# Kernel tuning notes

Hardware: AMD Instinct MI355X
Metric: run time of the kernel (lower is better)

Reference implementation:

```python
import jax, jax.numpy as jnp
import numpy as np

V, E, H, L, T, B = 30522, 256, 256, 512, 64, 128
EOS = 2


def setup_inputs() -> dict:
    key = jax.random.key(0)
    ks = jax.random.split(key, 16)
    s = 0.05
    return {
        "z": jax.random.normal(ks[0], (B, L), jnp.float32),
        "target_seq": jax.random.randint(ks[1], (B, T), 0, V, jnp.int64),
        "emb": jax.random.normal(ks[2], (V, E), jnp.float32) * s,
        "W_ih0": jax.random.normal(ks[3], (4 * H, E), jnp.float32) * s,
        "W_hh0": jax.random.normal(ks[4], (4 * H, H), jnp.float32) * s,
        "b_ih0": jax.random.normal(ks[5], (4 * H,), jnp.float32) * s,
        "b_hh0": jax.random.normal(ks[6], (4 * H,), jnp.float32) * s,
        "W_ih1": jax.random.normal(ks[7], (4 * H, H), jnp.float32) * s,
        "W_hh1": jax.random.normal(ks[8], (4 * H, H), jnp.float32) * s,
        "b_ih1": jax.random.normal(ks[9], (4 * H,), jnp.float32) * s,
        "b_hh1": jax.random.normal(ks[10], (4 * H,), jnp.float32) * s,
        "W_out": jax.random.normal(ks[11], (V, H), jnp.float32) * s,
        "b_out": jax.random.normal(ks[12], (V,), jnp.float32) * s,
        "W_lat": jax.random.normal(ks[13], (H, L), jnp.float32) * s,
        "b_lat": jax.random.normal(ks[14], (H,), jnp.float32) * s,
    }


def _lstm_cell(x, h, c, W_ih, W_hh, b_ih, b_hh):
    # PyTorch gate order: i, f, g, o
    gates = x @ W_ih.T + b_ih + h @ W_hh.T + b_hh  # [B, 4H]
    i, f, g, o = jnp.split(gates, 4, axis=-1)
    i, f, o = jax.nn.sigmoid(i), jax.nn.sigmoid(f), jax.nn.sigmoid(o)
    g = jnp.tanh(g)
    c_new = f * c + i * g
    h_new = o * jnp.tanh(c_new)
    return h_new, c_new


def reference(z, target_seq, emb, W_ih0, W_hh0, b_ih0, b_hh0,
              W_ih1, W_hh1, b_ih1, b_hh1, W_out, b_out, W_lat, b_lat):
    batch = z.shape[0]
    # initial hidden from latent, repeated per layer; cell zeros
    h_init = z @ W_lat.T + b_lat  # [B, H]
    c_init = jnp.zeros_like(h_init)
    # teacher-forced input tokens: [EOS, target[:, :-1]]
    tok = jnp.concatenate(
        [jnp.full((batch, 1), EOS, target_seq.dtype), target_seq[:, :-1]], axis=1)
    xs = emb[tok]  # [B, T, E]
    xs = jnp.transpose(xs, (1, 0, 2))  # [T, B, E]

    def step(carry, x_t):
        h0, c0, h1, c1 = carry
        h0, c0 = _lstm_cell(x_t, h0, c0, W_ih0, W_hh0, b_ih0, b_hh0)
        h1, c1 = _lstm_cell(h0, h1, c1, W_ih1, W_hh1, b_ih1, b_hh1)
        return (h0, c0, h1, c1), h1

    _, hs = jax.lax.scan(step, (h_init, c_init, h_init, c_init), xs)  # [T, B, H]
    logits = jnp.einsum('tbh,vh->btv', hs, W_out) + b_out  # [B, T, V]
    return logits
```

## Files before the change

### kernel.cpp

```cpp
#include <hip/hip_runtime.h>
#include <hip/hip_bf16.h>

#define B_ 128
#define T_ 64
#define H_ 256
#define E_ 256
#define L_ 512
#define V_ 30522
#define EOS_ 2
#define BH_ (B_ * H_)

typedef __attribute__((ext_vector_type(8))) short bf16x8;
typedef __attribute__((ext_vector_type(4))) float f32x4;

__device__ __forceinline__ float4 ld4(const float* p) { return *(const float4*)p; }
__device__ __forceinline__ float dot4(float4 a, float4 b) {
  return a.x * b.x + a.y * b.y + a.z * b.z + a.w * b.w;
}
__device__ __forceinline__ float sigf(float x) {
  return __builtin_amdgcn_rcpf(1.f + __expf(-x));
}
__device__ __forceinline__ float tanh_fast(float x) {
  float e = __expf(2.f * x);
  return 1.f - 2.f * __builtin_amdgcn_rcpf(e + 1.f);
}
__device__ __forceinline__ f32x4 mfma16(bf16x8 a, bf16x8 b, f32x4 c) {
  return __builtin_amdgcn_mfma_f32_16x16x32_bf16(a, b, c, 0, 0, 0);
}

__global__ __launch_bounds__(256) void conv_all(
    const float* __restrict__ emb, const float* __restrict__ w0i,
    const float* __restrict__ w0h, const float* __restrict__ w1i,
    const float* __restrict__ w1h, const float* __restrict__ wout,
    __hip_bfloat16* __restrict__ dEmb, __hip_bfloat16* __restrict__ dW0i,
    __hip_bfloat16* __restrict__ dW0h, __hip_bfloat16* __restrict__ dW1i,
    __hip_bfloat16* __restrict__ dW1h, __hip_bfloat16* __restrict__ dWout) {
  long i = ((long)blockIdx.x * 256 + threadIdx.x) * 8;
  const float* src; __hip_bfloat16* dst; long off;
  if (i < 7813632L)       { src = emb;  dst = dEmb;  off = i; }
  else if (i < 8075776L)  { src = w0i;  dst = dW0i;  off = i - 7813632L; }
  else if (i < 8337920L)  { src = w0h;  dst = dW0h;  off = i - 8075776L; }
  else if (i < 8600064L)  { src = w1i;  dst = dW1i;  off = i - 8337920L; }
  else if (i < 8862208L)  { src = w1h;  dst = dW1h;  off = i - 8600064L; }
  else if (i < 16675840L) { src = wout; dst = dWout; off = i - 8862208L; }
  else return;
  float4 lo = ld4(src + off), hi = ld4(src + off + 4);
  union { bf16x8 v8; __hip_bfloat16 e[8]; } u;
  u.e[0] = __float2bfloat16(lo.x); u.e[1] = __float2bfloat16(lo.y);
  u.e[2] = __float2bfloat16(lo.z); u.e[3] = __float2bfloat16(lo.w);
  u.e[4] = __float2bfloat16(hi.x); u.e[5] = __float2bfloat16(hi.y);
  u.e[6] = __float2bfloat16(hi.z); u.e[7] = __float2bfloat16(hi.w);
  *(bf16x8*)(dst + off) = u.v8;
}

__global__ __launch_bounds__(256) void reset_cnt(int* __restrict__ c) {
  int i = blockIdx.x * 256 + threadIdx.x;
  if (i < 8448) c[i] = 0;
}

__global__ __launch_bounds__(256) void init_kernel(
    const float* __restrict__ z, const float* __restrict__ W_lat,
    const float* __restrict__ b_lat,
    __hip_bfloat16* __restrict__ h0hi, __hip_bfloat16* __restrict__ h0res,
    __hip_bfloat16* __restrict__ hshi, __hip_bfloat16* __restrict__ hsres) {
  int b = blockIdx.x;
  int h = threadIdx.x;
  const float* zr = z + (size_t)b * L_;
  const float* wr = W_lat + (size_t)h * L_;
  float acc = b_lat[h];
  #pragma unroll 4
  for (int l = 0; l < L_; l += 4) acc += dot4(ld4(zr + l), ld4(wr + l));
  __hip_bfloat16 hi = __float2bfloat16(acc);
  __hip_bfloat16 re = __float2bfloat16(acc - __bfloat162float(hi));
  int idx = b * H_ + h;
  h0hi[idx] = hi; h0res[idx] = re;
  hshi[idx] = hi; hsres[idx] = re;
}

__global__ __launch_bounds__(256, 1) void lstm_persist(
    const int* __restrict__ targ, const __hip_bfloat16* __restrict__ embB,
    const __hip_bfloat16* __restrict__ Wih0B, const __hip_bfloat16* __restrict__ Whh0B,
    const float* __restrict__ b_ih0, const float* __restrict__ b_hh0,
    const __hip_bfloat16* __restrict__ Wih1B, const __hip_bfloat16* __restrict__ Whh1B,
    const float* __restrict__ b_ih1, const float* __restrict__ b_hh1,
    __hip_bfloat16* __restrict__ h0hi, __hip_bfloat16* __restrict__ h0res,
    __hip_bfloat16* __restrict__ hshi, __hip_bfloat16* __restrict__ hsres,
    int* __restrict__ flags, int* __restrict__ tickets) {
  __shared__ int role_sh;
  __shared__ int gang_sh;
  if (threadIdx.x == 0) {
    unsigned xcd;
    asm volatile("s_getreg_b32 %0, hwreg(HW_REG_XCC_ID)" : "=s"(xcd));
    xcd &= 7u;
    role_sh = __hip_atomic_fetch_add(tickets + xcd * 32, 1, __ATOMIC_RELAXED,
                                     __HIP_MEMORY_SCOPE_AGENT);
    gang_sh = (int)xcd;
  }
  __syncthreads();
  const int role = role_sh;
  if (role >= 32) return;
  const int gang = gang_sh;
  const bool isL0 = role < 16;
  const int chunk = role & 15;

  int* flag0 = flags + gang * 1024;
  int* flag1 = flag0 + 512;

  const int tid = threadIdx.x;
  const int lane = tid & 63;
  const int wave = tid >> 6;
  const int arow = lane & 15;
  const int klo = lane >> 4;
  const int hcol = chunk * 16 + arow;
  const int brow0 = gang * 16;
  const int myrow = brow0 + arow;

  const __hip_bfloat16* W1 = isL0 ? Wih0B : Wih1B;
  const __hip_bfloat16* W2 = isL0 ? Whh0B : Whh1B;
  bf16x8 bw1[8], bw2[8];
  {
    const size_t wrow = (size_t)(wave * 256 + hcol) * 256;
    #pragma unroll
    for (int ks = 0; ks < 8; ++ks) {
      bw1[ks] = *(const bf16x8*)(W1 + wrow + ks * 32 + klo * 8);
      bw2[ks] = *(const bf16x8*)(W2 + wrow + ks * 32 + klo * 8);
    }
  }

  const int erow = tid >> 4;
  const int ecol = tid & 15;
  const float* bi = isL0 ? b_ih0 : b_ih1;
  const float* bh = isL0 ? b_hh0 : b_hh1;
  const int ehcol = chunk * 16 + ecol;
  const float bias_i = bi[ehcol] + bh[ehcol];
  const float bias_f = bi[256 + ehcol] + bh[256 + ehcol];
  const float bias_g = bi[512 + ehcol] + bh[512 + ehcol];
  const float bias_o = bi[768 + ehcol] + bh[768 + ehcol];
  float c_state = 0.f;

  __shared__ float glds[4][16][17];

  for (int t = 0; t < T_; ++t) {
    {
      const int need0 = isL0 ? t : t + 1;
      const int need1 = isL0 ? 0 : t;
      if (tid < 64) {
        int* p = nullptr; int need = 0;
        if (lane < 16) { p = flag0 + lane * 32; need = need0; }
        else if (lane < 32) { p = flag1 + (lane - 16) * 32; need = need1; }
        int it = 0;
        for (;;) {
          bool ok = true;
          if (p && need > 0) ok = (atomicAdd(p, 0) >= need);
          if (__all(ok)) break;
          if (++it >= (1 << 14)) break;
          __builtin_amdgcn_s_sleep(1);
        }
      }
      __syncthreads();
    }

    f32x4 acc0 = (f32x4){0.f, 0.f, 0.f, 0.f};
    f32x4 acc1 = (f32x4){0.f, 0.f, 0.f, 0.f};
    if (isL0) {
      int tok = (t == 0) ? EOS_ : targ[myrow * T_ + t - 1];
      const __hip_bfloat16* xp = embB + (size_t)tok * E_;
      const __hip_bfloat16* hhp = h0hi + (size_t)t * BH_ + myrow * H_;
      const __hip_bfloat16* hrp = h0res + (size_t)t * BH_ + myrow * H_;
      #pragma unroll
      for (int ks = 0; ks < 8; ++ks) {
        const int ko = ks * 32 + klo * 8;
        bf16x8 ax = *(const bf16x8*)(xp + ko);
        bf16x8 ahh = *(const bf16x8*)(hhp + ko);
        bf16x8 ahr = *(const bf16x8*)(hrp + ko);
        if (ks & 1) {
          acc1 = mfma16(ax, bw1[ks], acc1);
          acc1 = mfma16(ahh, bw2[ks], acc1);
          acc1 = mfma16(ahr, bw2[ks], acc1);
        } else {
          acc0 = mfma16(ax, bw1[ks], acc0);
          acc0 = mfma16(ahh, bw2[ks], acc0);
          acc0 = mfma16(ahr, bw2[ks], acc0);
        }
      }
    } else {
      const __hip_bfloat16* xhp = h0hi + (size_t)(t + 1) * BH_ + myrow * H_;
      const __hip_bfloat16* xrp = h0res + (size_t)(t + 1) * BH_ + myrow * H_;
      const __hip_bfloat16* hhp = hshi + (size_t)t * BH_ + myrow * H_;
      const __hip_bfloat16* hrp = hsres + (size_t)t * BH_ + myrow * H_;
      #pragma unroll
      for (int ks = 0; ks < 8; ++ks) {
        const int ko = ks * 32 + klo * 8;
        bf16x8 axh = *(const bf16x8*)(xhp + ko);
        bf16x8 axr = *(const bf16x8*)(xrp + ko);
        bf16x8 ahh = *(const bf16x8*)(hhp + ko);
        bf16x8 ahr = *(const bf16x8*)(hrp + ko);
        if (ks & 1) {
          acc1 = mfma16(axh, bw1[ks], acc1);
          acc1 = mfma16(axr, bw1[ks], acc1);
          acc1 = mfma16(ahh, bw2[ks], acc1);
          acc1 = mfma16(ahr, bw2[ks], acc1);
        } else {
          acc0 = mfma16(axh, bw1[ks], acc0);
          acc0 = mfma16(axr, bw1[ks], acc0);
          acc0 = mfma16(ahh, bw2[ks], acc0);
          acc0 = mfma16(ahr, bw2[ks], acc0);
        }
      }
    }
    #pragma unroll
    for (int r = 0; r < 4; ++r)
      glds[wave][klo * 4 + r][arow] = acc0[r] + acc1[r];
    __syncthreads();

    {
      float gi = glds[0][erow][ecol] + bias_i;
      float gf = glds[1][erow][ecol] + bias_f;
      float gg = glds[2][erow][ecol] + bias_g;
      float go = glds[3][erow][ecol] + bias_o;
      float iv = sigf(gi), fv = sigf(gf), gv = tanh_fast(gg), ov = sigf(go);
      c_state = fv * c_state + iv * gv;
      float h = ov * tanh_fast(c_state);
      __hip_bfloat16 hi = __float2bfloat16(h);
      __hip_bfloat16 re = __float2bfloat16(h - __bfloat162float(hi));
      size_t off = (size_t)(t + 1) * BH_ + (size_t)(brow0 + erow) * H_ + ehcol;
      (isL0 ? h0hi : hshi)[off] = hi;
      (isL0 ? h0res : hsres)[off] = re;
    }

    __syncthreads();
    if (tid == 0) atomicAdd((isL0 ? flag0 : flag1) + chunk * 32, 1);
  }
}

__global__ __launch_bounds__(256) void gemm_out(
    const __hip_bfloat16* __restrict__ hs,
    const __hip_bfloat16* __restrict__ Wb, const float* __restrict__ bout,
    float* __restrict__ out) {
  __shared__ __hip_bfloat16 ldsA[2][128 * 32];
  __shared__ __hip_bfloat16 ldsB[2][128 * 32];

  const int tid = threadIdx.x;
  const int lane = tid & 63;
  const int wave = tid >> 6;
  const int wr = wave >> 1, wc = wave & 1;
  const int m0 = blockIdx.x * 128;
  const int n0 = blockIdx.y * 128;
  const int row_in = lane & 15;
  const int kgrp = lane >> 4;

  auto stage = [&](int kb, int buf) {
    #pragma unroll
    for (int p = 0; p < 2; ++p) {
      int slot = p * 256 + wave * 64 + lane;
      int row = slot >> 2;
      int kd = ((slot & 3) + (row >> 1)) & 3;
      const __hip_bfloat16* srcA = hs + (size_t)(m0 + row) * H_ + kb * 32 + kd * 8;
      int rn = n0 + row; if (rn >= V_) rn = V_ - 1;
      const __hip_bfloat16* srcB = Wb + (size_t)rn * H_ + kb * 32 + kd * 8;
      __hip_bfloat16* dstA = &ldsA[buf][0] + (p * 2048 + wave * 512);
      __hip_bfloat16* dstB = &ldsB[buf][0] + (p * 2048 + wave * 512);
      __builtin_amdgcn_global_load_lds(
          (const __attribute__((address_space(1))) unsigned int*)srcA,
          (__attribute__((address_space(3))) unsigned int*)dstA, 16, 0, 0);
      __builtin_amdgcn_global_load_lds(
          (const __attribute__((address_space(1))) unsigned int*)srcB,
          (__attribute__((address_space(3))) unsigned int*)dstB, 16, 0, 0);
    }
  };

  f32x4 acc[4][4];
  #pragma unroll
  for (int i = 0; i < 4; ++i)
    #pragma unroll
    for (int j = 0; j < 4; ++j) acc[i][j] = (f32x4){0.f, 0.f, 0.f, 0.f};

  stage(0, 0);
  __syncthreads();

  int buf = 0;
  for (int kb = 0; kb < 8; ++kb) {
    if (kb < 7) stage(kb + 1, buf ^ 1);
    bf16x8 a[4], b[4];
    #pragma unroll
    for (int mi = 0; mi < 4; ++mi) {
      int row = wr * 64 + mi * 16 + row_in;
      int g = (kgrp - (row >> 1)) & 3;
      a[mi] = *(const bf16x8*)(&ldsA[buf][0] + row * 32 + g * 8);
    }
    #pragma unroll
    for (int ni = 0; ni < 4; ++ni) {
      int row = wc * 64 + ni * 16 + row_in;
      int g = (kgrp - (row >> 1)) & 3;
      b[ni] = *(const bf16x8*)(&ldsB[buf][0] + row * 32 + g * 8);
    }
    #pragma unroll
    for (int mi = 0; mi < 4; ++mi)
      #pragma unroll
      for (int ni = 0; ni < 4; ++ni)
        acc[mi][ni] = mfma16(a[mi], b[ni], acc[mi][ni]);
    __syncthreads();
    buf ^= 1;
  }

  #pragma unroll
  for (int ni = 0; ni < 4; ++ni) {
    int v = n0 + wc * 64 + ni * 16 + row_in;
    if (v >= V_) continue;
    float bias = bout[v];
    #pragma unroll
    for (int mi = 0; mi < 4; ++mi) {
      #pragma unroll
      for (int r = 0; r < 4; ++r) {
        int m = m0 + wr * 64 + mi * 16 + kgrp * 4 + r;
        int tt = m >> 7;
        int bb_ = m & 127;
        out[((size_t)bb_ * T_ + tt) * V_ + v] = acc[mi][ni][r] + bias;
      }
    }
  }
}

extern "C" void kernel_launch(void* const* d_in, const int* in_sizes, int n_in,
                              void* d_out, int out_size, void* d_ws, size_t ws_size,
                              hipStream_t stream) {
  const float* z     = (const float*)d_in[0];
  const int*   targ  = (const int*)d_in[1];
  const float* emb   = (const float*)d_in[2];
  const float* W_ih0 = (const float*)d_in[3];
  const float* W_hh0 = (const float*)d_in[4];
  const float* b_ih0 = (const float*)d_in[5];
  const float* b_hh0 = (const float*)d_in[6];
  const float* W_ih1 = (const float*)d_in[7];
  const float* W_hh1 = (const float*)d_in[8];
  const float* b_ih1 = (const float*)d_in[9];
  const float* b_hh1 = (const float*)d_in[10];
  const float* W_out = (const float*)d_in[11];
  const float* b_out = (const float*)d_in[12];
  const float* W_lat = (const float*)d_in[13];
  const float* b_lat = (const float*)d_in[14];
  float* out = (float*)d_out;

  char* ws = (char*)d_ws;
  __hip_bfloat16* h0hi  = (__hip_bfloat16*)(ws);
  __hip_bfloat16* h0res = (__hip_bfloat16*)(ws + 4259840);
  __hip_bfloat16* hshi  = (__hip_bfloat16*)(ws + 8519680);
  __hip_bfloat16* hsres = (__hip_bfloat16*)(ws + 12779520);
  __hip_bfloat16* embB  = (__hip_bfloat16*)(ws + 17039360);
  __hip_bfloat16* Wih0B = (__hip_bfloat16*)(ws + 32666624);
  __hip_bfloat16* Whh0B = (__hip_bfloat16*)(ws + 33190912);
  __hip_bfloat16* Wih1B = (__hip_bfloat16*)(ws + 33715200);
  __hip_bfloat16* Whh1B = (__hip_bfloat16*)(ws + 34239488);
  __hip_bfloat16* WoutB = (__hip_bfloat16*)(ws + 34763776);
  int* flags = (int*)(ws + 50391040);
  int* tickets = flags + 8192;

  reset_cnt<<<33, 256, 0, stream>>>(flags);
  conv_all<<<8144, 256, 0, stream>>>(emb, W_ih0, W_hh0, W_ih1, W_hh1, W_out,
                                     embB, Wih0B, Whh0B, Wih1B, Whh1B, WoutB);
  init_kernel<<<128, 256, 0, stream>>>(z, W_lat, b_lat, h0hi, h0res, hshi, hsres);

  lstm_persist<<<512, 256, 0, stream>>>(
      targ, embB,
      Wih0B, Whh0B, b_ih0, b_hh0,
      Wih1B, Whh1B, b_ih1, b_hh1,
      h0hi, h0res, hshi, hsres, flags, tickets);

  {
    dim3 g(64, 239);
    gemm_out<<<g, 256, 0, stream>>>(hshi + BH_, WoutB, b_out, out);
  }
}
```

Measured before the change: 1.055 ms.

## Fuse LSTM recurrence and output projection into one persistent kernel with flag-gated tiles

Merges the persistent LSTM kernel and the vocabulary projection GEMM into a single launch. Blocks beyond the 32 recurrence roles per XCD pull output tiles from a per-XCD work queue, each tile covering 8 timesteps by 16 batch rows by 128 vocab columns. Before computing, a tile spin-waits on per-timestep completion counters that the layer-1 blocks increment. This lets the large logits GEMM overlap the serial recurrence instead of running after it. In exchange it adds spin-waiting, sharing of compute units with the latency-critical recurrence blocks, and a dependence on enough blocks being co-resident.

Result: faster. 950.7 us (-9.9%).

```diff
diff --git a/kernel.cpp b/kernel.cpp
--- a/kernel.cpp
+++ b/kernel.cpp
@@ -9,6 +9,8 @@
 #define V_ 30522
 #define EOS_ 2
 #define BH_ (B_ * H_)
+#define NTILE_N 239
+#define TILES_PER_XCD (8 * NTILE_N)
 
 typedef __attribute__((ext_vector_type(8))) short bf16x8;
 typedef __attribute__((ext_vector_type(4))) float f32x4;
@@ -55,7 +57,7 @@
 
 __global__ __launch_bounds__(256) void reset_cnt(int* __restrict__ c) {
   int i = blockIdx.x * 256 + threadIdx.x;
-  if (i < 8448) c[i] = 0;
+  if (i < 25088) c[i] = 0;
 }
 
 __global__ __launch_bounds__(256) void init_kernel(
@@ -77,7 +79,7 @@
   hshi[idx] = hi; hsres[idx] = re;
 }
 
-__global__ __launch_bounds__(256, 1) void lstm_persist(
+__global__ __launch_bounds__(256, 3) void fused(
     const int* __restrict__ targ, const __hip_bfloat16* __restrict__ embB,
     const __hip_bfloat16* __restrict__ Wih0B, const __hip_bfloat16* __restrict__ Whh0B,
     const float* __restrict__ b_ih0, const float* __restrict__ b_hh0,
@@ -85,10 +87,15 @@
     const float* __restrict__ b_ih1, const float* __restrict__ b_hh1,
     __hip_bfloat16* __restrict__ h0hi, __hip_bfloat16* __restrict__ h0res,
     __hip_bfloat16* __restrict__ hshi, __hip_bfloat16* __restrict__ hsres,
-    int* __restrict__ flags, int* __restrict__ tickets) {
-  __shared__ int role_sh;
-  __shared__ int gang_sh;
-  if (threadIdx.x == 0) {
+    const __hip_bfloat16* __restrict__ Wb, const float* __restrict__ bout,
+    float* __restrict__ out,
+    int* __restrict__ flags, int* __restrict__ tickets,
+    int* __restrict__ gqx, int* __restrict__ hsdone_g) {
+  __shared__ int role_sh, gang_sh, tile_sh;
+  __shared__ char smem[32768];
+
+  const int tid = threadIdx.x;
+  if (tid == 0) {
     unsigned xcd;
     asm volatile("s_getreg_b32 %0, hwreg(HW_REG_XCC_ID)" : "=s"(xcd));
     xcd &= 7u;
@@ -98,224 +105,244 @@
   }
   __syncthreads();
   const int role = role_sh;
-  if (role >= 32) return;
   const int gang = gang_sh;
-  const bool isL0 = role < 16;
-  const int chunk = role & 15;
-
-  int* flag0 = flags + gang * 1024;
-  int* flag1 = flag0 + 512;
-
-  const int tid = threadIdx.x;
   const int lane = tid & 63;
-  const int wave = tid >> 6;
-  const int arow = lane & 15;
-  const int klo = lane >> 4;
-  const int hcol = chunk * 16 + arow;
-  const int brow0 = gang * 16;
-  const int myrow = brow0 + arow;
-
-  const __hip_bfloat16* W1 = isL0 ? Wih0B : Wih1B;
-  const __hip_bfloat16* W2 = isL0 ? Whh0B : Whh1B;
-  bf16x8 bw1[8], bw2[8];
-  {
-    const size_t wrow = (size_t)(wave * 256 + hcol) * 256;
-    #pragma unroll
-    for (int ks = 0; ks < 8; ++ks) {
-      bw1[ks] = *(const bf16x8*)(W1 + wrow + ks * 32 + klo * 8);
-      bw2[ks] = *(const bf16x8*)(W2 + wrow + ks * 32 + klo * 8);
+
+  if (role < 32) {
+    const bool isL0 = role < 16;
+    const int chunk = role & 15;
+    int* flag0 = flags + gang * 1024;
+    int* flag1 = flag0 + 512;
+
+    const int wave = tid >> 6;
+    const int arow = lane & 15;
+    const int klo = lane >> 4;
+    const int hcol = chunk * 16 + arow;
+    const int brow0 = gang * 16;
+    const int myrow = brow0 + arow;
+
+    const __hip_bfloat16* W1 = isL0 ? Wih0B : Wih1B;
+    const __hip_bfloat16* W2 = isL0 ? Whh0B : Whh1B;
+    bf16x8 bw1[8], bw2[8];
+    {
+      const size_t wrow = (size_t)(wave * 256 + hcol) * 256;
+      #pragma unroll
+      for (int ks = 0; ks < 8; ++ks) {
+        bw1[ks] = *(const bf16x8*)(W1 + wrow + ks * 32 + klo * 8);
+        bw2[ks] = *(const bf16x8*)(W2 + wrow + ks * 32 + klo * 8);
+      }
+    }
+
+    const int erow = tid >> 4;
+    const int ecol = tid & 15;
+    const float* bi = isL0 ? b_ih0 : b_ih1;
+    const float* bh = isL0 ? b_hh0 : b_hh1;
+    const int ehcol = chunk * 16 + ecol;
+    const float bias_i = bi[ehcol] + bh[ehcol];
+    const float bias_f = bi[256 + ehcol] + bh[256 + ehcol];
+    const float bias_g = bi[512 + ehcol] + bh[512 + ehcol];
+    const float bias_o = bi[768 + ehcol] + bh[768 + ehcol];
+    float c_state = 0.f;
+
+    typedef float GL[16][17];
+    GL* glds = (GL*)smem;
+
+    for (int t = 0; t < T_; ++t) {
+      {
+        const int need0 = isL0 ? t : t + 1;
+        const int need1 = isL0 ? 0 : t;
+        if (tid < 64) {
+          int* p = nullptr; int need = 0;
+          if (lane < 16) { p = flag0 + lane * 32; need = need0; }
+          else if (lane < 32) { p = flag1 + (lane - 16) * 32; need = need1; }
+          int it = 0;
+          for (;;) {
+            bool ok = true;
+            if (p && need > 0) ok = (atomicAdd(p, 0) >= need);
+            if (__all(ok)) break;
+            if (++it >= (1 << 15)) break;
+            __builtin_amdgcn_s_sleep(1);
+          }
+        }
+        __syncthreads();
+      }
+
+      f32x4 acc0 = (f32x4){0.f, 0.f, 0.f, 0.f};
+      f32x4 acc1 = (f32x4){0.f, 0.f, 0.f, 0.f};
+      if (isL0) {
+        int tok = (t == 0) ? EOS_ : targ[myrow * T_ + t - 1];
+        const __hip_bfloat16* xp = embB + (size_t)tok * E_;
+        const __hip_bfloat16* hhp = h0hi + (size_t)t * BH_ + myrow * H_;
+        const __hip_bfloat16* hrp = h0res + (size_t)t * BH_ + myrow * H_;
+        #pragma unroll
+        for (int ks = 0; ks < 8; ++ks) {
+          const int ko = ks * 32 + klo * 8;
+          bf16x8 ax = *(const bf16x8*)(xp + ko);
+          bf16x8 ahh = *(const bf16x8*)(hhp + ko);
+          bf16x8 ahr = *(const bf16x8*)(hrp + ko);
+          if (ks & 1) {
+            acc1 = mfma16(ax, bw1[ks], acc1);
+            acc1 = mfma16(ahh, bw2[ks], acc1);
+            acc1 = mfma16(ahr, bw2[ks], acc1);
+          } else {
+            acc0 = mfma16(ax, bw1[ks], acc0);
+            acc0 = mfma16(ahh, bw2[ks], acc0);
+            acc0 = mfma16(ahr, bw2[ks], acc0);
+          }
+        }
+      } else {
+        const __hip_bfloat16* xhp = h0hi + (size_t)(t + 1) * BH_ + myrow * H_;
+        const __hip_bfloat16* xrp = h0res + (size_t)(t + 1) * BH_ + myrow * H_;
+        const __hip_bfloat16* hhp = hshi + (size_t)t * BH_ + myrow * H_;
+        const __hip_bfloat16* hrp = hsres + (size_t)t * BH_ + myrow * H_;
+        #pragma unroll
+        for (int ks = 0; ks < 8; ++ks) {
+          const int ko = ks * 32 + klo * 8;
+          bf16x8 axh = *(const bf16x8*)(xhp + ko);
+          bf16x8 axr = *(const bf16x8*)(xrp + ko);
+          bf16x8 ahh = *(const bf16x8*)(hhp + ko);
+          bf16x8 ahr = *(const bf16x8*)(hrp + ko);
+          if (ks & 1) {
+            acc1 = mfma16(axh, bw1[ks], acc1);
+            acc1 = mfma16(axr, bw1[ks], acc1);
+            acc1 = mfma16(ahh, bw2[ks], acc1);
+            acc1 = mfma16(ahr, bw2[ks], acc1);
+          } else {
+            acc0 = mfma16(axh, bw1[ks], acc0);
+            acc0 = mfma16(axr, bw1[ks], acc0);
+            acc0 = mfma16(ahh, bw2[ks], acc0);
+            acc0 = mfma16(ahr, bw2[ks], acc0);
+          }
+        }
+      }
+      #pragma unroll
+      for (int r = 0; r < 4; ++r)
+        glds[tid >> 6][klo * 4 + r][arow] = acc0[r] + acc1[r];
+      __syncthreads();
+
+      {
+        float gi = glds[0][erow][ecol] + bias_i;
+        float gf = glds[1][erow][ecol] + bias_f;
+        float gg = glds[2][erow][ecol] + bias_g;
+        float go = glds[3][erow][ecol] + bias_o;
+        float iv = sigf(gi), fv = sigf(gf), gv = tanh_fast(gg), ov = sigf(go);
+        c_state = fv * c_state + iv * gv;
+        float h = ov * tanh_fast(c_state);
+        __hip_bfloat16 hi = __float2bfloat16(h);
+        __hip_bfloat16 re = __float2bfloat16(h - __bfloat162float(hi));
+        size_t off = (size_t)(t + 1) * BH_ + (size_t)(brow0 + erow) * H_ + ehcol;
+        (isL0 ? h0hi : hshi)[off] = hi;
+        (isL0 ? h0res : hsres)[off] = re;
+      }
+
+      __syncthreads();
+      if (tid == 0) {
+        atomicAdd((isL0 ? flag0 : flag1) + chunk * 32, 1);
+        if (!isL0) atomicAdd(hsdone_g + (gang * 64 + t) * 32, 1);
+      }
     }
   }
 
-  const int erow = tid >> 4;
-  const int ecol = tid & 15;
-  const float* bi = isL0 ? b_ih0 : b_ih1;
-  const float* bh = isL0 ? b_hh0 : b_hh1;
-  const int ehcol = chunk * 16 + ecol;
-  const float bias_i = bi[ehcol] + bh[ehcol];
-  const float bias_f = bi[256 + ehcol] + bh[256 + ehcol];
-  const float bias_g = bi[512 + ehcol] + bh[512 + ehcol];
-  const float bias_o = bi[768 + ehcol] + bh[768 + ehcol];
-  float c_state = 0.f;
-
-  __shared__ float glds[4][16][17];
-
-  for (int t = 0; t < T_; ++t) {
-    {
-      const int need0 = isL0 ? t : t + 1;
-      const int need1 = isL0 ? 0 : t;
-      if (tid < 64) {
-        int* p = nullptr; int need = 0;
-        if (lane < 16) { p = flag0 + lane * 32; need = need0; }
-        else if (lane < 32) { p = flag1 + (lane - 16) * 32; need = need1; }
-        int it = 0;
-        for (;;) {
-          bool ok = true;
-          if (p && need > 0) ok = (atomicAdd(p, 0) >= need);
-          if (__all(ok)) break;
-          if (++it >= (1 << 14)) break;
-          __builtin_amdgcn_s_sleep(1);
-        }
-      }
-      __syncthreads();
-    }
-
-    f32x4 acc0 = (f32x4){0.f, 0.f, 0.f, 0.f};
-    f32x4 acc1 = (f32x4){0.f, 0.f, 0.f, 0.f};
-    if (isL0) {
-      int tok = (t == 0) ? EOS_ : targ[myrow * T_ + t - 1];
-      const __hip_bfloat16* xp = embB + (size_t)tok * E_;
-      const __hip_bfloat16* hhp = h0hi + (size_t)t * BH_ + myrow * H_;
-      const __hip_bfloat16* hrp = h0res + (size_t)t * BH_ + myrow * H_;
-      #pragma unroll
-      for (int ks = 0; ks < 8; ++ks) {
-        const int ko = ks * 32 + klo * 8;
-        bf16x8 ax = *(const bf16x8*)(xp + ko);
-        bf16x8 ahh = *(const bf16x8*)(hhp + ko);
-        bf16x8 ahr = *(const bf16x8*)(hrp + ko);
-        if (ks & 1) {
-          acc1 = mfma16(ax, bw1[ks], acc1);
-          acc1 = mfma16(ahh, bw2[ks], acc1);
-          acc1 = mfma16(ahr, bw2[ks], acc1);
-        } else {
-          acc0 = mfma16(ax, bw1[ks], acc0);
-          acc0 = mfma16(ahh, bw2[ks], acc0);
-          acc0 = mfma16(ahr, bw2[ks], acc0);
-        }
-      }
-    } else {
-      const __hip_bfloat16* xhp = h0hi + (size_t)(t + 1) * BH_ + myrow * H_;
-      const __hip_bfloat16* xrp = h0res + (size_t)(t + 1) * BH_ + myrow * H_;
-      const __hip_bfloat16* hhp = hshi + (size_t)t * BH_ + myrow * H_;
-      const __hip_bfloat16* hrp = hsres + (size_t)t * BH_ + myrow * H_;
-      #pragma unroll
-      for (int ks = 0; ks < 8; ++ks) {
-        const int ko = ks * 32 + klo * 8;
-        bf16x8 axh = *(const bf16x8*)(xhp + ko);
-        bf16x8 axr = *(const bf16x8*)(xrp + ko);
-        bf16x8 ahh = *(const bf16x8*)(hhp + ko);
-        bf16x8 ahr = *(const bf16x8*)(hrp + ko);
-        if (ks & 1) {
-          acc1 = mfma16(axh, bw1[ks], acc1);
-          acc1 = mfma16(axr, bw1[ks], acc1);
-          acc1 = mfma16(ahh, bw2[ks], acc1);
-          acc1 = mfma16(ahr, bw2[ks], acc1);
-        } else {
-          acc0 = mfma16(axh, bw1[ks], acc0);
-          acc0 = mfma16(axr, bw1[ks], acc0);
-          acc0 = mfma16(ahh, bw2[ks], acc0);
-          acc0 = mfma16(ahr, bw2[ks], acc0);
-        }
-      }
-    }
-    #pragma unroll
-    for (int r = 0; r < 4; ++r)
-      glds[wave][klo * 4 + r][arow] = acc0[r] + acc1[r];
-    __syncthreads();
-
-    {
-      float gi = glds[0][erow][ecol] + bias_i;
-      float gf = glds[1][erow][ecol] + bias_f;
-      float gg = glds[2][erow][ecol] + bias_g;
-      float go = glds[3][erow][ecol] + bias_o;
-      float iv = sigf(gi), fv = sigf(gf), gv = tanh_fast(gg), ov = sigf(go);
-      c_state = fv * c_state + iv * gv;
-      float h = ov * tanh_fast(c_state);
-      __hip_bfloat16 hi = __float2bfloat16(h);
-      __hip_bfloat16 re = __float2bfloat16(h - __bfloat162float(hi));
-      size_t off = (size_t)(t + 1) * BH_ + (size_t)(brow0 + erow) * H_ + ehcol;
-      (isL0 ? h0hi : hshi)[off] = hi;
-      (isL0 ? h0res : hsres)[off] = re;
-    }
-
-    __syncthreads();
-    if (tid == 0) atomicAdd((isL0 ? flag0 : flag1) + chunk * 32, 1);
-  }
-}
-
-__global__ __launch_bounds__(256) void gemm_out(
-    const __hip_bfloat16* __restrict__ hs,
-    const __hip_bfloat16* __restrict__ Wb, const float* __restrict__ bout,
-    float* __restrict__ out) {
-  __shared__ __hip_bfloat16 ldsA[2][128 * 32];
-  __shared__ __hip_bfloat16 ldsB[2][128 * 32];
-
-  const int tid = threadIdx.x;
-  const int lane = tid & 63;
+  __hip_bfloat16* ldsA = (__hip_bfloat16*)smem;
+  __hip_bfloat16* ldsB = (__hip_bfloat16*)(smem + 16384);
   const int wave = tid >> 6;
   const int wr = wave >> 1, wc = wave & 1;
-  const int m0 = blockIdx.x * 128;
-  const int n0 = blockIdx.y * 128;
   const int row_in = lane & 15;
   const int kgrp = lane >> 4;
 
-  auto stage = [&](int kb, int buf) {
+  for (;;) {
+    if (tid == 0) tile_sh = atomicAdd(gqx + gang * 32, 1);
+    __syncthreads();
+    const int tau = tile_sh;
+    if (tau >= TILES_PER_XCD) return;
+    const int sg = tau / NTILE_N;
+    const int nt = tau - sg * NTILE_N;
+    const int n0 = nt * 128;
+    const int t0 = sg * 8;
+
+    if (tid < 64) {
+      const int* p = (lane < 8) ? hsdone_g + (gang * 64 + t0 + lane) * 32 : nullptr;
+      int it = 0;
+      for (;;) {
+        bool ok = true;
+        if (p) ok = (atomicAdd((int*)p, 0) >= 16);
+        if (__all(ok)) break;
+        if (++it >= (1 << 16)) break;
+        __builtin_amdgcn_s_sleep(8);
+      }
+    }
+    __syncthreads();
+
+    auto stage = [&](int kb, int buf) {
+      #pragma unroll
+      for (int p = 0; p < 2; ++p) {
+        int slot = p * 256 + wave * 64 + lane;
+        int row = slot >> 2;
+        int kd = ((slot & 3) + (row >> 1)) & 3;
+        const __hip_bfloat16* srcA =
+            hshi + (size_t)(t0 + (row >> 4) + 1) * BH_ +
+            (size_t)(gang * 16 + (row & 15)) * H_ + kb * 32 + kd * 8;
+        int rn = n0 + row; if (rn >= V_) rn = V_ - 1;
+        const __hip_bfloat16* srcB = Wb + (size_t)rn * H_ + kb * 32 + kd * 8;
+        __hip_bfloat16* dstA = ldsA + buf * 4096 + (p * 2048 + wave * 512);
+        __hip_bfloat16* dstB = ldsB + buf * 4096 + (p * 2048 + wave * 512);
+        __builtin_amdgcn_global_load_lds(
+            (const __attribute__((address_space(1))) unsigned int*)srcA,
+            (__attribute__((address_space(3))) unsigned int*)dstA, 16, 0, 0);
+        __builtin_amdgcn_global_load_lds(
+            (const __attribute__((address_space(1))) unsigned int*)srcB,
+            (__attribute__((address_space(3))) unsigned int*)dstB, 16, 0, 0);
+      }
+    };
+
+    f32x4 acc[4][4];
     #pragma unroll
-    for (int p = 0; p < 2; ++p) {
-      int slot = p * 256 + wave * 64 + lane;
-      int row = slot >> 2;
-      int kd = ((slot & 3) + (row >> 1)) & 3;
-      const __hip_bfloat16* srcA = hs + (size_t)(m0 + row) * H_ + kb * 32 + kd * 8;
-      int rn = n0 + row; if (rn >= V_) rn = V_ - 1;
-      const __hip_bfloat16* srcB = Wb + (size_t)rn * H_ + kb * 32 + kd * 8;
-      __hip_bfloat16* dstA = &ldsA[buf][0] + (p * 2048 + wave * 512);
-      __hip_bfloat16* dstB = &ldsB[buf][0] + (p * 2048 + wave * 512);
-      __builtin_amdgcn_global_load_lds(
-          (const __attribute__((address_space(1))) unsigned int*)srcA,
-          (__attribute__((address_space(3))) unsigned int*)dstA, 16, 0, 0);
-      __builtin_amdgcn_global_load_lds(
-          (const __attribute__((address_space(1))) unsigned int*)srcB,
-          (__attribute__((address_space(3))) unsigned int*)dstB, 16, 0, 0);
-    }
-  };
-
-  f32x4 acc[4][4];
-  #pragma unroll
-  for (int i = 0; i < 4; ++i)
-    #pragma unroll
-    for (int j = 0; j < 4; ++j) acc[i][j] = (f32x4){0.f, 0.f, 0.f, 0.f};
-
-  stage(0, 0);
-  __syncthreads();
-
-  int buf = 0;
-  for (int kb = 0; kb < 8; ++kb) {
-    if (kb < 7) stage(kb + 1, buf ^ 1);
-    bf16x8 a[4], b[4];
-    #pragma unroll
-    for (int mi = 0; mi < 4; ++mi) {
-      int row = wr * 64 + mi * 16 + row_in;
-      int g = (kgrp - (row >> 1)) & 3;
-      a[mi] = *(const bf16x8*)(&ldsA[buf][0] + row * 32 + g * 8);
-    }
+    for (int i = 0; i < 4; ++i)
+      #pragma unroll
+      for (int j = 0; j < 4; ++j) acc[i][j] = (f32x4){0.f, 0.f, 0.f, 0.f};
+
+    stage(0, 0);
+    __syncthreads();
+
+    int buf = 0;
+    for (int kb = 0; kb < 8; ++kb) {
+      if (kb < 7) stage(kb + 1, buf ^ 1);
+      bf16x8 a[4], b[4];
+      #pragma unroll
+      for (int mi = 0; mi < 4; ++mi) {
+        int row = wr * 64 + mi * 16 + row_in;
+        int g = (kgrp - (row >> 1)) & 3;
+        a[mi] = *(const bf16x8*)(ldsA + buf * 4096 + row * 32 + g * 8);
+      }
+      #pragma unroll
+      for (int ni = 0; ni < 4; ++ni) {
+        int row = wc * 64 + ni * 16 + row_in;
+        int g = (kgrp - (row >> 1)) & 3;
+        b[ni] = *(const bf16x8*)(ldsB + buf * 4096 + row * 32 + g * 8);
+      }
+      #pragma unroll
+      for (int mi = 0; mi < 4; ++mi)
+        #pragma unroll
+        for (int ni = 0; ni < 4; ++ni)
+          acc[mi][ni] = mfma16(a[mi], b[ni], acc[mi][ni]);
+      __syncthreads();
+      buf ^= 1;
+    }
+
     #pragma unroll
     for (int ni = 0; ni < 4; ++ni) {
-      int row = wc * 64 + ni * 16 + row_in;
-      int g = (kgrp - (row >> 1)) & 3;
-      b[ni] = *(const bf16x8*)(&ldsB[buf][0] + row * 32 + g * 8);
-    }
-    #pragma unroll
-    for (int mi = 0; mi < 4; ++mi)
-      #pragma unroll
-      for (int ni = 0; ni < 4; ++ni)
-        acc[mi][ni] = mfma16(a[mi], b[ni], acc[mi][ni]);
-    __syncthreads();
-    buf ^= 1;
-  }
-
-  #pragma unroll
-  for (int ni = 0; ni < 4; ++ni) {
-    int v = n0 + wc * 64 + ni * 16 + row_in;
-    if (v >= V_) continue;
-    float bias = bout[v];
-    #pragma unroll
-    for (int mi = 0; mi < 4; ++mi) {
-      #pragma unroll
-      for (int r = 0; r < 4; ++r) {
-        int m = m0 + wr * 64 + mi * 16 + kgrp * 4 + r;
-        int tt = m >> 7;
-        int bb_ = m & 127;
-        out[((size_t)bb_ * T_ + tt) * V_ + v] = acc[mi][ni][r] + bias;
+      int v = n0 + wc * 64 + ni * 16 + row_in;
+      if (v >= V_) continue;
+      float bias = bout[v];
+      #pragma unroll
+      for (int mi = 0; mi < 4; ++mi) {
+        #pragma unroll
+        for (int r = 0; r < 4; ++r) {
+          int m = wr * 64 + mi * 16 + kgrp * 4 + r;
+          int tt = t0 + (m >> 4);
+          int bb_ = gang * 16 + (m & 15);
+          out[((size_t)bb_ * T_ + tt) * V_ + v] = acc[mi][ni][r] + bias;
+        }
       }
     }
   }
@@ -352,22 +379,21 @@
   __hip_bfloat16* Wih1B = (__hip_bfloat16*)(ws + 33715200);
   __hip_bfloat16* Whh1B = (__hip_bfloat16*)(ws + 34239488);
   __hip_bfloat16* WoutB = (__hip_bfloat16*)(ws + 34763776);
-  int* flags = (int*)(ws + 50391040);
-  int* tickets = flags + 8192;
-
-  reset_cnt<<<33, 256, 0, stream>>>(flags);
+  int* flags    = (int*)(ws + 50391040);
+  int* tickets  = flags + 8192;
+  int* gqx      = flags + 8448;
+  int* hsdone_g = flags + 8704;
+
+  reset_cnt<<<98, 256, 0, stream>>>(flags);
   conv_all<<<8144, 256, 0, stream>>>(emb, W_ih0, W_hh0, W_ih1, W_hh1, W_out,
                                      embB, Wih0B, Whh0B, Wih1B, Whh1B, WoutB);
   init_kernel<<<128, 256, 0, stream>>>(z, W_lat, b_lat, h0hi, h0res, hshi, hsres);
 
-  lstm_persist<<<512, 256, 0, stream>>>(
+  fused<<<768, 256, 0, stream>>>(
       targ, embB,
       Wih0B, Whh0B, b_ih0, b_hh0,
       Wih1B, Whh1B, b_ih1, b_hh1,
-      h0hi, h0res, hshi, hsres, flags, tickets);
-
-  {
-    dim3 g(64, 239);
-    gemm_out<<<g, 256, 0, stream>>>(hshi + BH_, WoutB, b_out, out);
-  }
-}
+      h0hi, h0res, hshi, hsres,
+      WoutB, b_out, out,
+      flags, tickets, gqx, hsdone_g);
+}
```
